# Kernel tuning notes

Measured on AMD Instinct MI355X. Metric: run time of the kernel, lower is better.

## Reference

```python
import jax, jax.numpy as jnp
import numpy as np

N_BITS = 8  # total bit-width of the slice method [1,1,2,2,2]


def _quantize(t, bits=N_BITS):
    """Symmetric per-tensor fixed-point quantize->dequantize.

    This is the ideal recombination of SlicedData bit slices: the engine's
    MapReduceDot computes per-slice partial dot products and reduces them
    with powers-of-two weights, which (absent analog noise) is exactly a
    dot product of the fixed-point-quantized operands.
    """
    qmax = 2.0 ** (bits - 1) - 1.0
    scale = jnp.maximum(jnp.max(jnp.abs(t)) / qmax, 1e-12)
    return jnp.round(t / scale) * scale


def setup_inputs() -> dict:
    key = jax.random.key(0)
    k1, k2 = jax.random.split(key)
    B, D, N = 1024, 512, 16384
    x = jax.random.normal(k1, (B, D), dtype=jnp.float32)
    weight = jax.random.normal(k2, (D, N), dtype=jnp.float32)  # one vector per column
    return {"x": x, "weight": weight, "split_square_len": 32}


def reference(x, weight, split_square_len):
    B, D = x.shape
    N = weight.shape[1]
    L = split_square_len
    # bias = sum(y^2) / L, replicated L rows and stacked below the weight
    bias = jnp.sum(weight * weight, axis=0) / L            # [N]
    bias_rows = jnp.broadcast_to(bias, (L, N))             # [L, N]
    temp = jnp.concatenate([weight, bias_rows], axis=0)    # [D+L, N]
    # input padded with ones so the bias rows accumulate to sum(y^2)
    x_pad = jnp.concatenate([x, jnp.ones((B, L), dtype=x.dtype)], axis=1)  # [B, D+L]
    # MapReduceDot: bit-sliced fixed-point dot product (ideal recombination)
    out = jnp.dot(_quantize(x_pad), _quantize(temp))       # [B, N] = x@W + ||y||^2
    return out
```

## Files before the change

### kernel.cpp

```cpp
#include <hip/hip_runtime.h>
#include <hip/hip_bf16.h>

#define B_DIM 1024
#define D_DIM 512
#define N_DIM 16384

typedef __attribute__((ext_vector_type(8))) short bf16x8;
typedef __attribute__((ext_vector_type(4))) float f32x4;

#define IDX_XPART 16
#define IDX_WPART 256
#define OFF_BIAS  4096
#define OFF_XQ    69632
#define OFF_WQT   1118208

#define XMAX_BLOCKS 128
#define WSTAT_BLOCKS 256
#define QX_BLOCKS 512

__device__ inline void gload16(const void* g, void* l) {
  __builtin_amdgcn_global_load_lds((const __attribute__((address_space(1))) void*)g,
                                   (__attribute__((address_space(3))) void*)l, 16, 0, 0);
}

__device__ inline unsigned short f2bf(float f) {
  return (unsigned short)(__float_as_uint(f) >> 16);
}

__device__ inline void compute_scales(const float* __restrict__ ws_f, int lane,
                                      float& sx, float& st, float& s, float& q1) {
  float xm = fmaxf(ws_f[IDX_XPART + lane], ws_f[IDX_XPART + 64 + lane]);
  float wm = fmaxf(fmaxf(ws_f[IDX_WPART + lane], ws_f[IDX_WPART + 64 + lane]),
                   fmaxf(ws_f[IDX_WPART + 128 + lane], ws_f[IDX_WPART + 192 + lane]));
  #pragma unroll
  for (int i = 1; i < 64; i <<= 1) {
    xm = fmaxf(xm, __shfl_xor(xm, i, 64));
    wm = fmaxf(wm, __shfl_xor(wm, i, 64));
  }
  st = fmaxf(wm / 127.0f, 1e-12f);
  sx = fmaxf(fmaxf(xm, 1.0f) / 127.0f, 1e-12f);
  s = sx * st;
  q1 = rintf(1.0f / sx);
}

__global__ __launch_bounds__(256) void k_stats(const float* __restrict__ x,
                                               const float* __restrict__ w,
                                               float* __restrict__ ws_f) {
  const int t = threadIdx.x;
  if (blockIdx.x < XMAX_BLOCKS) {
    __shared__ float red[256];
    float m = 0.f;
    const float4* x4 = (const float4*)x;
    const int n4 = B_DIM * D_DIM / 4;
    for (int i = blockIdx.x * 256 + t; i < n4; i += XMAX_BLOCKS * 256) {
      float4 v = x4[i];
      m = fmaxf(m, fmaxf(fmaxf(fabsf(v.x), fabsf(v.y)), fmaxf(fabsf(v.z), fabsf(v.w))));
    }
    red[t] = m; __syncthreads();
    for (int s = 128; s > 0; s >>= 1) { if (t < s) red[t] = fmaxf(red[t], red[t + s]); __syncthreads(); }
    if (t == 0) ws_f[IDX_XPART + blockIdx.x] = red[0];
  } else {
    __shared__ float sred[256], mred[256];
    const int b = blockIdx.x - XMAX_BLOCKS;
    const int c = t & 63, part = t >> 6;
    const int col = b * 64 + c;
    float ss = 0.f, mx = 0.f;
    const float* p = w + (size_t)part * 128 * N_DIM + col;
    #pragma unroll 8
    for (int d = 0; d < 128; ++d) {
      float v = p[(size_t)d * N_DIM];
      ss += v * v;
      mx = fmaxf(mx, fabsf(v));
    }
    sred[t] = ss; mred[t] = mx;
    __syncthreads();
    if (t < 64) {
      float bsum = (sred[t] + sred[t + 64] + sred[t + 128] + sred[t + 192]) * (1.0f / 32.0f);
      ws_f[OFF_BIAS / 4 + col] = bsum;
      mred[t] = fmaxf(mred[t], bsum);
    }
    __syncthreads();
    for (int s = 128; s > 0; s >>= 1) { if (t < s) mred[t] = fmaxf(mred[t], mred[t + s]); __syncthreads(); }
    if (t == 0) ws_f[IDX_WPART + b] = mred[0];
  }
}

__global__ __launch_bounds__(256) void k_quant(const float* __restrict__ x,
                                               const float* __restrict__ w,
                                               const float* __restrict__ ws_f,
                                               unsigned short* __restrict__ xq,
                                               unsigned short* __restrict__ wqT) {
  const int t = threadIdx.x;
  float sx, st, s_u, q1_u;
  compute_scales(ws_f, t & 63, sx, st, s_u, q1_u);
  if (blockIdx.x < QX_BLOCKS) {
    const int i = blockIdx.x * 256 + t;
    float4 v = ((const float4*)x)[i];
    ushort4 o;
    o.x = f2bf(rintf(v.x / sx));
    o.y = f2bf(rintf(v.y / sx));
    o.z = f2bf(rintf(v.z / sx));
    o.w = f2bf(rintf(v.w / sx));
    ((ushort4*)xq)[i] = o;
  } else {
    __shared__ float tile[64][65];
    const int bid = blockIdx.x - QX_BLOCKS;
    const int n0 = (bid & 255) * 64, k0 = (bid >> 8) * 64;
    {
      const int tx = t & 63, ty = t >> 6;
      #pragma unroll
      for (int i = 0; i < 16; ++i) {
        int r = i * 4 + ty;
        tile[r][tx] = w[(size_t)(k0 + r) * N_DIM + n0 + tx];
      }
    }
    __syncthreads();
    const int kg = t & 15, nr = t >> 4;
    #pragma unroll
    for (int it = 0; it < 4; ++it) {
      const int nl = it * 16 + nr;
      ushort4 o;
      o.x = f2bf(rintf(tile[kg * 4 + 0][nl] / st));
      o.y = f2bf(rintf(tile[kg * 4 + 1][nl] / st));
      o.z = f2bf(rintf(tile[kg * 4 + 2][nl] / st));
      o.w = f2bf(rintf(tile[kg * 4 + 3][nl] / st));
      *(ushort4*)&wqT[(size_t)(n0 + nl) * D_DIM + k0 + kg * 4] = o;
    }
  }
}

#define NT 16

__device__ inline void stage4(const unsigned short* __restrict__ xq,
                              const unsigned short* __restrict__ wqT,
                              int m0, int n0, int kbase, short* buf, int w, int lane) {
  #pragma unroll
  for (int i = 0; i < 2; ++i) {
    const int r0 = w * 32 + i * 16;
    const int rl = r0 + (lane >> 2);
    const int kc = (lane & 3) ^ ((lane >> 2) & 3);
    gload16(xq + (size_t)(m0 + rl) * D_DIM + kbase + kc * 8, buf + r0 * 32);
    gload16(wqT + (size_t)(n0 + rl) * D_DIM + kbase + kc * 8, buf + 4096 + r0 * 32);
  }
}

__global__ __launch_bounds__(256, 3) void k_gemm(const unsigned short* __restrict__ xq,
                                                 const unsigned short* __restrict__ wqT,
                                                 const float* __restrict__ bias,
                                                 const float* __restrict__ ws_f,
                                                 float* __restrict__ out) {
  __shared__ __align__(16) short lds[3 * 8192];
  const int t = threadIdx.x;
  const int lane = t & 63, w = t >> 6;
  const int wm = w >> 1, wn = w & 1;
  const int nid = (blockIdx.x & 7) * 128 + (blockIdx.x >> 3);
  const int m0 = (nid & 7) * 128;
  const int n0 = (nid >> 3) * 128;

  stage4(xq, wqT, m0, n0, 0, &lds[0], w, lane);
  stage4(xq, wqT, m0, n0, 32, &lds[8192], w, lane);
  float sx_u, st, s, q1;
  compute_scales(ws_f, lane, sx_u, st, s, q1);

  f32x4 acc[4][4] = {};

  asm volatile("s_waitcnt vmcnt(4)" ::: "memory");
  __builtin_amdgcn_s_barrier();
  __builtin_amdgcn_sched_barrier(0);

  for (int T = 0; T < NT; ++T) {
    short* buf = &lds[(T % 3) * 8192];
    bf16x8 af[4], bfr[4];
    #pragma unroll
    for (int f = 0; f < 4; ++f) {
      const int ra = wm * 64 + f * 16 + (lane & 15);
      af[f] = *(const bf16x8*)&buf[ra * 32 + (((lane >> 4) ^ (ra & 3))) * 8];
      const int rb = wn * 64 + f * 16 + (lane & 15);
      bfr[f] = *(const bf16x8*)&buf[4096 + rb * 32 + (((lane >> 4) ^ (rb & 3))) * 8];
    }
    if (T + 2 < NT)
      stage4(xq, wqT, m0, n0, (T + 2) * 32, &lds[((T + 2) % 3) * 8192], w, lane);
    __builtin_amdgcn_s_setprio(1);
    #pragma unroll
    for (int fm = 0; fm < 4; ++fm)
      #pragma unroll
      for (int fn = 0; fn < 4; ++fn)
        acc[fm][fn] = __builtin_amdgcn_mfma_f32_16x16x32_bf16(af[fm], bfr[fn], acc[fm][fn], 0, 0, 0);
    __builtin_amdgcn_s_setprio(0);
    if (T + 2 < NT)      asm volatile("s_waitcnt vmcnt(4)" ::: "memory");
    else if (T + 1 < NT) asm volatile("s_waitcnt vmcnt(0)" ::: "memory");
    if (T + 1 < NT) __builtin_amdgcn_s_barrier();
    __builtin_amdgcn_sched_barrier(0);
  }

  #pragma unroll
  for (int fn = 0; fn < 4; ++fn) {
    const int col = n0 + wn * 64 + fn * 16 + (lane & 15);
    const float ba = 32.0f * q1 * rintf(bias[col] / st);
    #pragma unroll
    for (int fm = 0; fm < 4; ++fm) {
      const int rbase = m0 + wm * 64 + fm * 16 + ((lane >> 4) * 4);
      #pragma unroll
      for (int r = 0; r < 4; ++r)
        out[(size_t)(rbase + r) * N_DIM + col] = (acc[fm][fn][r] + ba) * s;
    }
  }
}

extern "C" void kernel_launch(void* const* d_in, const int* in_sizes, int n_in,
                              void* d_out, int out_size, void* d_ws, size_t ws_size,
                              hipStream_t stream) {
  const float* x = (const float*)d_in[0];
  const float* w = (const float*)d_in[1];
  float* out = (float*)d_out;
  char* ws = (char*)d_ws;
  float* ws_f = (float*)ws;
  float* bias = (float*)(ws + OFF_BIAS);
  unsigned short* xq = (unsigned short*)(ws + OFF_XQ);
  unsigned short* wqT = (unsigned short*)(ws + OFF_WQT);

  hipLaunchKernelGGL(k_stats, dim3(XMAX_BLOCKS + WSTAT_BLOCKS), dim3(256), 0, stream, x, w, ws_f);
  hipLaunchKernelGGL(k_quant, dim3(QX_BLOCKS + 2048), dim3(256), 0, stream, x, w, ws_f, xq, wqT);
  hipLaunchKernelGGL(k_gemm, dim3((B_DIM / 128) * (N_DIM / 128)), dim3(256), 0, stream,
                     xq, wqT, bias, ws_f, out);
}
```

Before: 46.79 us.

## Switch quantized GEMM from bf16 MFMA to int8 MFMA with packed operands

Quantized x and transposed weight are stored as packed int8 instead of bf16-encoded integers, which halves the intermediate buffers and the GEMM load traffic. The GEMM now uses the i32 16x16x64 int8 MFMA with a 64-wide K step, taking 8 iterations instead of 16. The pipeline changes from triple to double buffering with a full vmcnt(0) wait and barrier each iteration, and occupancy is raised to 4 blocks. Exactness depends on quantized values fitting in [-127,127], which the per-tensor scaling guarantees. The simpler pipeline may expose more load latency per iteration.

```diff
diff --git a/kernel.cpp b/kernel.cpp
--- a/kernel.cpp
+++ b/kernel.cpp
@@ -5,14 +5,14 @@
 #define D_DIM 512
 #define N_DIM 16384
 
-typedef __attribute__((ext_vector_type(8))) short bf16x8;
+typedef __attribute__((ext_vector_type(4))) int   i32x4;
 typedef __attribute__((ext_vector_type(4))) float f32x4;
 
 #define IDX_XPART 16
 #define IDX_WPART 256
 #define OFF_BIAS  4096
 #define OFF_XQ    69632
-#define OFF_WQT   1118208
+#define OFF_WQT   593920
 
 #define XMAX_BLOCKS 128
 #define WSTAT_BLOCKS 256
@@ -21,10 +21,6 @@
 __device__ inline void gload16(const void* g, void* l) {
   __builtin_amdgcn_global_load_lds((const __attribute__((address_space(1))) void*)g,
                                    (__attribute__((address_space(3))) void*)l, 16, 0, 0);
-}
-
-__device__ inline unsigned short f2bf(float f) {
-  return (unsigned short)(__float_as_uint(f) >> 16);
 }
 
 __device__ inline void compute_scales(const float* __restrict__ ws_f, int lane,
@@ -85,27 +81,30 @@
   }
 }
 
+__device__ inline unsigned pack4(float a, float b, float c, float d, float inv) {
+  int q0 = (int)rintf(a * inv), q1 = (int)rintf(b * inv);
+  int q2 = (int)rintf(c * inv), q3 = (int)rintf(d * inv);
+  return (q0 & 255) | ((q1 & 255) << 8) | ((q2 & 255) << 16) | ((unsigned)(q3 & 255) << 24);
+}
+
 __global__ __launch_bounds__(256) void k_quant(const float* __restrict__ x,
                                                const float* __restrict__ w,
                                                const float* __restrict__ ws_f,
-                                               unsigned short* __restrict__ xq,
-                                               unsigned short* __restrict__ wqT) {
+                                               unsigned* __restrict__ xq,
+                                               unsigned* __restrict__ wqT) {
   const int t = threadIdx.x;
   float sx, st, s_u, q1_u;
   compute_scales(ws_f, t & 63, sx, st, s_u, q1_u);
   if (blockIdx.x < QX_BLOCKS) {
     const int i = blockIdx.x * 256 + t;
+    const float inv = 1.0f / sx;
     float4 v = ((const float4*)x)[i];
-    ushort4 o;
-    o.x = f2bf(rintf(v.x / sx));
-    o.y = f2bf(rintf(v.y / sx));
-    o.z = f2bf(rintf(v.z / sx));
-    o.w = f2bf(rintf(v.w / sx));
-    ((ushort4*)xq)[i] = o;
+    xq[i] = pack4(v.x, v.y, v.z, v.w, inv);
   } else {
     __shared__ float tile[64][65];
     const int bid = blockIdx.x - QX_BLOCKS;
     const int n0 = (bid & 255) * 64, k0 = (bid >> 8) * 64;
+    const float inv = 1.0f / st;
     {
       const int tx = t & 63, ty = t >> 6;
       #pragma unroll
@@ -119,37 +118,33 @@
     #pragma unroll
     for (int it = 0; it < 4; ++it) {
       const int nl = it * 16 + nr;
-      ushort4 o;
-      o.x = f2bf(rintf(tile[kg * 4 + 0][nl] / st));
-      o.y = f2bf(rintf(tile[kg * 4 + 1][nl] / st));
-      o.z = f2bf(rintf(tile[kg * 4 + 2][nl] / st));
-      o.w = f2bf(rintf(tile[kg * 4 + 3][nl] / st));
-      *(ushort4*)&wqT[(size_t)(n0 + nl) * D_DIM + k0 + kg * 4] = o;
-    }
-  }
-}
-
-#define NT 16
-
-__device__ inline void stage4(const unsigned short* __restrict__ xq,
-                              const unsigned short* __restrict__ wqT,
-                              int m0, int n0, int kbase, short* buf, int w, int lane) {
+      wqT[((size_t)(n0 + nl) * D_DIM + k0 + kg * 4) >> 2] =
+          pack4(tile[kg * 4 + 0][nl], tile[kg * 4 + 1][nl],
+                tile[kg * 4 + 2][nl], tile[kg * 4 + 3][nl], inv);
+    }
+  }
+}
+
+#define NT 8
+
+__device__ inline void stage(const char* __restrict__ xq, const char* __restrict__ wqT,
+                             int m0, int n0, int kbase, char* buf, int w, int lane) {
+  const int rl = lane >> 2;
+  const int kc = ((lane & 3) ^ (rl & 3)) * 16;
   #pragma unroll
   for (int i = 0; i < 2; ++i) {
     const int r0 = w * 32 + i * 16;
-    const int rl = r0 + (lane >> 2);
-    const int kc = (lane & 3) ^ ((lane >> 2) & 3);
-    gload16(xq + (size_t)(m0 + rl) * D_DIM + kbase + kc * 8, buf + r0 * 32);
-    gload16(wqT + (size_t)(n0 + rl) * D_DIM + kbase + kc * 8, buf + 4096 + r0 * 32);
-  }
-}
-
-__global__ __launch_bounds__(256, 3) void k_gemm(const unsigned short* __restrict__ xq,
-                                                 const unsigned short* __restrict__ wqT,
+    gload16(xq + (size_t)(m0 + r0 + rl) * D_DIM + kbase + kc, buf + r0 * 64);
+    gload16(wqT + (size_t)(n0 + r0 + rl) * D_DIM + kbase + kc, buf + 8192 + r0 * 64);
+  }
+}
+
+__global__ __launch_bounds__(256, 4) void k_gemm(const char* __restrict__ xq,
+                                                 const char* __restrict__ wqT,
                                                  const float* __restrict__ bias,
                                                  const float* __restrict__ ws_f,
                                                  float* __restrict__ out) {
-  __shared__ __align__(16) short lds[3 * 8192];
+  __shared__ __align__(16) char lds[2 * 16384];
   const int t = threadIdx.x;
   const int lane = t & 63, w = t >> 6;
   const int wm = w >> 1, wn = w & 1;
@@ -157,39 +152,33 @@
   const int m0 = (nid & 7) * 128;
   const int n0 = (nid >> 3) * 128;
 
-  stage4(xq, wqT, m0, n0, 0, &lds[0], w, lane);
-  stage4(xq, wqT, m0, n0, 32, &lds[8192], w, lane);
+  stage(xq, wqT, m0, n0, 0, &lds[0], w, lane);
   float sx_u, st, s, q1;
   compute_scales(ws_f, lane, sx_u, st, s, q1);
 
-  f32x4 acc[4][4] = {};
-
-  asm volatile("s_waitcnt vmcnt(4)" ::: "memory");
-  __builtin_amdgcn_s_barrier();
-  __builtin_amdgcn_sched_barrier(0);
+  i32x4 acc[4][4] = {};
 
   for (int T = 0; T < NT; ++T) {
-    short* buf = &lds[(T % 3) * 8192];
-    bf16x8 af[4], bfr[4];
+    char* buf = &lds[(T & 1) * 16384];
+    asm volatile("s_waitcnt vmcnt(0)" ::: "memory");
+    __builtin_amdgcn_s_barrier();
+    if (T + 1 < NT)
+      stage(xq, wqT, m0, n0, (T + 1) * 64, &lds[((T + 1) & 1) * 16384], w, lane);
+    i32x4 af[4], bfr[4];
     #pragma unroll
     for (int f = 0; f < 4; ++f) {
       const int ra = wm * 64 + f * 16 + (lane & 15);
-      af[f] = *(const bf16x8*)&buf[ra * 32 + (((lane >> 4) ^ (ra & 3))) * 8];
+      af[f] = *(const i32x4*)&buf[ra * 64 + (((lane >> 4) ^ (ra & 3))) * 16];
       const int rb = wn * 64 + f * 16 + (lane & 15);
-      bfr[f] = *(const bf16x8*)&buf[4096 + rb * 32 + (((lane >> 4) ^ (rb & 3))) * 8];
-    }
-    if (T + 2 < NT)
-      stage4(xq, wqT, m0, n0, (T + 2) * 32, &lds[((T + 2) % 3) * 8192], w, lane);
+      bfr[f] = *(const i32x4*)&buf[8192 + rb * 64 + (((lane >> 4) ^ (rb & 3))) * 16];
+    }
     __builtin_amdgcn_s_setprio(1);
     #pragma unroll
     for (int fm = 0; fm < 4; ++fm)
       #pragma unroll
       for (int fn = 0; fn < 4; ++fn)
-        acc[fm][fn] = __builtin_amdgcn_mfma_f32_16x16x32_bf16(af[fm], bfr[fn], acc[fm][fn], 0, 0, 0);
+        acc[fm][fn] = __builtin_amdgcn_mfma_i32_16x16x64_i8(af[fm], bfr[fn], acc[fm][fn], 0, 0, 0);
     __builtin_amdgcn_s_setprio(0);
-    if (T + 2 < NT)      asm volatile("s_waitcnt vmcnt(4)" ::: "memory");
-    else if (T + 1 < NT) asm volatile("s_waitcnt vmcnt(0)" ::: "memory");
-    if (T + 1 < NT) __builtin_amdgcn_s_barrier();
     __builtin_amdgcn_sched_barrier(0);
   }
 
@@ -202,7 +191,7 @@
       const int rbase = m0 + wm * 64 + fm * 16 + ((lane >> 4) * 4);
       #pragma unroll
       for (int r = 0; r < 4; ++r)
-        out[(size_t)(rbase + r) * N_DIM + col] = (acc[fm][fn][r] + ba) * s;
+        out[(size_t)(rbase + r) * N_DIM + col] = ((float)acc[fm][fn][r] + ba) * s;
     }
   }
 }
@@ -216,11 +205,12 @@
   char* ws = (char*)d_ws;
   float* ws_f = (float*)ws;
   float* bias = (float*)(ws + OFF_BIAS);
-  unsigned short* xq = (unsigned short*)(ws + OFF_XQ);
-  unsigned short* wqT = (unsigned short*)(ws + OFF_WQT);
+  char* xq = ws + OFF_XQ;
+  char* wqT = ws + OFF_WQT;
 
   hipLaunchKernelGGL(k_stats, dim3(XMAX_BLOCKS + WSTAT_BLOCKS), dim3(256), 0, stream, x, w, ws_f);
-  hipLaunchKernelGGL(k_quant, dim3(QX_BLOCKS + 2048), dim3(256), 0, stream, x, w, ws_f, xq, wqT);
+  hipLaunchKernelGGL(k_quant, dim3(QX_BLOCKS + 2048), dim3(256), 0, stream, x, w, ws_f,
+                     (unsigned*)xq, (unsigned*)wqT);
   hipLaunchKernelGGL(k_gemm, dim3((B_DIM / 128) * (N_DIM / 128)), dim3(256), 0, stream,
                      xq, wqT, bias, ws_f, out);
 }
```

Measured after the change: 41.91 us. -10.4%, faster.
